# Optimization experiments

Measured on AMD Instinct MI355X. Metric: run time of the kernel, lower is better.

The kernel has to match this reference:

```python
import jax, jax.numpy as jnp
import numpy as np

N_NODES = 50000
N_EDGES = 800000
D_IN = 128
D_OUT = 128
N_MLP = 2


def _lin(x, W, b):
    return x @ W.T + b


def setup_inputs() -> dict:
    key = jax.random.key(0)
    ks = jax.random.split(key, 32)
    d = {}
    d['feat'] = jax.random.normal(ks[0], (N_NODES, D_IN), dtype=jnp.float32)
    d['src'] = jax.random.randint(ks[1], (N_EDGES,), 0, N_NODES, dtype=jnp.int32)
    d['dst'] = jax.random.randint(ks[2], (N_EDGES,), 0, N_NODES, dtype=jnp.int32)
    s_in = 1.0 / np.sqrt(D_IN)
    s_out = 1.0 / np.sqrt(D_OUT)
    i = 3
    def w(shape, s):
        nonlocal i
        out = jax.random.normal(ks[i], shape, dtype=jnp.float32) * s
        i += 1
        return out
    for nm in ['asrc', 'adst', 'asub', 'amul']:
        d['W_' + nm] = w((D_OUT, D_IN), s_in)
        d['b_' + nm] = w((D_OUT,), s_in)
    d['W_aout'] = w((1, D_OUT), s_out)
    d['b_aout'] = w((1,), s_out)
    for nm in ['pool', 'pool2']:
        d['W_' + nm] = w((D_IN, D_IN), s_in)
        d['b_' + nm] = w((D_IN,), s_in)
    for nm in ['self', 'neigh', 'neigh2']:
        d['W_' + nm] = w((D_OUT, D_IN), s_in)
        d['b_' + nm] = w((D_OUT,), s_in)
    d['W_mlp'] = w((N_MLP, D_OUT, D_OUT), s_out)
    d['b_mlp'] = w((N_MLP, D_OUT), s_out)
    return d


def reference(feat, src, dst,
              W_asrc, b_asrc, W_adst, b_adst, W_asub, b_asub, W_amul, b_amul,
              W_aout, b_aout, W_pool, b_pool, W_pool2, b_pool2,
              W_self, b_self, W_neigh, b_neigh, W_neigh2, b_neigh2,
              W_mlp, b_mlp):
    gelu = lambda x: jax.nn.gelu(x, approximate=False)
    fs = feat[src]            # [E, D_IN] gathered source feats
    fd = feat[dst]            # [E, D_IN] gathered dest feats
    # edge attention score
    e = _lin(fs - fd, W_asub, b_asub) + _lin(fs * fd, W_amul, b_amul)
    e = e + _lin(feat, W_asrc, b_asrc)[src] + _lin(feat, W_adst, b_adst)[dst]
    e = gelu(e)
    e = jax.nn.leaky_relu(_lin(e, W_aout, b_aout), 0.2)  # [E, 1]
    deg = jax.ops.segment_sum(jnp.ones((src.shape[0],), jnp.float32), dst,
                              num_segments=N_NODES)      # in-degree
    has_in = (deg > 0)[:, None]
    # max-pool branch
    h = gelu(_lin(feat, W_pool, b_pool))
    m = e * h[src]
    neigh = jax.ops.segment_max(m, dst, num_segments=N_NODES)
    neigh = jnp.where(has_in, neigh, 0.0)
    # mean-pool branch
    h2 = gelu(_lin(feat, W_pool2, b_pool2))
    m2 = e * h2[src]
    neigh2 = jax.ops.segment_sum(m2, dst, num_segments=N_NODES)
    neigh2 = neigh2 / jnp.maximum(deg, 1.0)[:, None]
    rst = _lin(feat, W_self, b_self) + _lin(neigh, W_neigh, b_neigh) \
        + _lin(neigh2, W_neigh2, b_neigh2)
    for li in range(W_mlp.shape[0]):
        rst = rst + _lin(gelu(rst), W_mlp[li], b_mlp[li])
    return rst
```

## Files before the change

### kernel.cpp

```cpp
#include <hip/hip_runtime.h>
#include <cstdint>
#include <cstddef>

#define NN 50000
#define NE 800000
#define DD 128

#define NBK 391
#define BSLOT 4096

static_assert(NN % 16 == 0, "node tiles");
static_assert(NE % 16 == 0, "edge tiles");
static_assert(((NN + 127) >> 7) == NBK, "bucket count");

typedef _Float16 h16_t;
typedef h16_t h16x8 __attribute__((ext_vector_type(8)));
typedef h16_t h16x4 __attribute__((ext_vector_type(4)));
typedef float f32x4 __attribute__((ext_vector_type(4)));
typedef float f32x16 __attribute__((ext_vector_type(16)));

__device__ __forceinline__ float gelu_f(float x) {
    float u = x * x;
    float t = fmaf(u, -0.1029442445f, -2.3021184019f);
    float s = __builtin_amdgcn_exp2f(x * t);
    return x * __builtin_amdgcn_rcpf(1.0f + s);
}

__device__ __forceinline__ int frag_idx(int ch, int k) {
    int t = ch >> 4, n = ch & 15;
    int kb = k >> 5, r = k & 31, q = r >> 3, j = r & 7;
    return ((((t * 4 + kb) * 4 + q) * 16 + n) << 3) + j;
}

__device__ __forceinline__ int frag32_idx(int ch, int k) {
    int t = ch >> 5, m = ch & 31;
    int kc = k >> 4, q = (k >> 3) & 1, j = k & 7;
    return ((((t * 8 + kc) * 2 + q) * 32 + m) << 3) + j;
}

__global__ __launch_bounds__(256) void convert_feat_kernel(
    const float* __restrict__ feat, h16_t* __restrict__ fb)
{
    int i = blockIdx.x * 256 + threadIdx.x;
    f32x4 v = ((const f32x4*)feat)[i];
    h16x4 o;
    o[0] = (h16_t)v[0]; o[1] = (h16_t)v[1]; o[2] = (h16_t)v[2]; o[3] = (h16_t)v[3];
    ((h16x4*)fb)[i] = o;
}

__global__ __launch_bounds__(256) void prep_kernel(
    const float* __restrict__ W_asrc, const float* __restrict__ b_asrc,
    const float* __restrict__ W_adst, const float* __restrict__ b_adst,
    const float* __restrict__ W_asub, const float* __restrict__ b_asub,
    const float* __restrict__ W_amul, const float* __restrict__ b_amul,
    const float* __restrict__ W_pool, const float* __restrict__ W_pool2,
    const float* __restrict__ W_self, const float* __restrict__ b_self,
    const float* __restrict__ W_neigh, const float* __restrict__ b_neigh,
    const float* __restrict__ W_neigh2, const float* __restrict__ b_neigh2,
    const float* __restrict__ W_mlp,
    h16_t* __restrict__ W_Sf, h16_t* __restrict__ W_Df, h16_t* __restrict__ W_amulf,
    h16_t* __restrict__ W_poolf, h16_t* __restrict__ W_pool2f,
    h16_t* __restrict__ W_selff, h16_t* __restrict__ W_neighf, h16_t* __restrict__ W_neigh2f,
    h16_t* __restrict__ W_mlpf,
    float* __restrict__ b_e, float* __restrict__ b_rst)
{
    int gid = blockIdx.x * 256 + threadIdx.x;
    float sub = W_asub[gid];
    int ch = gid >> 7, k = gid & 127;
    int fi = frag_idx(ch, k);
    W_Sf[fi] = (h16_t)(W_asrc[gid] + sub);
    W_Df[fi] = (h16_t)(W_adst[gid] - sub);
    W_amulf[frag32_idx(ch, k)] = (h16_t)W_amul[gid];
    W_poolf[fi]   = (h16_t)W_pool[gid];
    W_pool2f[fi]  = (h16_t)W_pool2[gid];
    W_selff[fi]   = (h16_t)W_self[gid];
    W_neighf[fi]  = (h16_t)W_neigh[gid];
    W_neigh2f[fi] = (h16_t)W_neigh2[gid];
    W_mlpf[fi]            = (h16_t)W_mlp[gid];
    W_mlpf[DD * DD + fi]  = (h16_t)W_mlp[DD * DD + gid];
    if (gid < DD) {
        b_e[gid]   = b_asub[gid] + b_amul[gid] + b_asrc[gid] + b_adst[gid];
        b_rst[gid] = b_self[gid] + b_neigh[gid] + b_neigh2[gid];
    }
}

__global__ __launch_bounds__(256) void scatter_bucket_kernel(
    const int* __restrict__ src, const int* __restrict__ dst,
    int* __restrict__ gcursor, int2* __restrict__ ebuf)
{
    __shared__ int cnt[NBK];
    __shared__ int ofs[NBK];
    int t = threadIdx.x;
    for (int b = t; b < NBK; b += 256) cnt[b] = 0;
    __syncthreads();
    int qbase = blockIdx.x * 1024 + t;
    int4 s4[4], d4[4];
    bool valid[4];
#pragma unroll
    for (int k = 0; k < 4; k++) {
        int q = qbase + k * 256;
        valid[k] = q < NE / 4;
        if (valid[k]) {
            s4[k] = ((const int4*)src)[q];
            d4[k] = ((const int4*)dst)[q];
#pragma unroll
            for (int j = 0; j < 4; j++)
                atomicAdd(&cnt[((&d4[k].x)[j]) >> 7], 1);
        }
    }
    __syncthreads();
    for (int b = t; b < NBK; b += 256) {
        int c = cnt[b];
        ofs[b] = c ? atomicAdd(&gcursor[b], c) : 0;
    }
    __syncthreads();
#pragma unroll
    for (int k = 0; k < 4; k++) {
        if (valid[k]) {
#pragma unroll
            for (int j = 0; j < 4; j++) {
                int d = (&d4[k].x)[j];
                int b = d >> 7;
                int p = atomicAdd(&ofs[b], 1);
                int2 pk;
                pk.x = (&s4[k].x)[j];
                pk.y = d;
                ebuf[(size_t)b * BSLOT + p] = pk;
            }
        }
    }
}

__global__ __launch_bounds__(512) void bucket_scan_kernel(
    const int* __restrict__ gcursor, int* __restrict__ boff)
{
    __shared__ int tmp[512];
    int t = threadIdx.x;
    int v = (t < NBK) ? gcursor[t] : 0;
    tmp[t] = v;
    __syncthreads();
#pragma unroll
    for (int d = 1; d < 512; d <<= 1) {
        int x = (t >= d) ? tmp[t - d] : 0;
        __syncthreads();
        tmp[t] += x;
        __syncthreads();
    }
    if (t < NBK) boff[t] = tmp[t] - v;
}

__global__ __launch_bounds__(256) void finalize_csr_kernel(
    const int2* __restrict__ ebuf, const int* __restrict__ gcursor, const int* __restrict__ boff,
    int2* __restrict__ csr, int* __restrict__ offsets, int* __restrict__ deg)
{
    __shared__ int lcnt[128];
    __shared__ int nbase[128];
    __shared__ int pre[128];
    int B = blockIdx.x, t = threadIdx.x;
    int v0 = B << 7;
    int cnt = gcursor[B];
    int dbase = boff[B];
    const int2* eb = ebuf + (size_t)B * BSLOT;
    if (t < 128) lcnt[t] = 0;
    __syncthreads();
    for (int i = t; i < cnt; i += 256)
        atomicAdd(&lcnt[eb[i].y - v0], 1);
    __syncthreads();
    int c = (t < 128) ? lcnt[t] : 0;
    if (t < 128) pre[t] = c;
    __syncthreads();
#pragma unroll
    for (int d = 1; d < 128; d <<= 1) {
        int x = (t >= d && t < 128) ? pre[t - d] : 0;
        __syncthreads();
        if (t < 128) pre[t] += x;
        __syncthreads();
    }
    if (t < 128) {
        int nb = dbase + pre[t] - c;
        nbase[t] = nb;
        int v = v0 + t;
        if (v < NN) { offsets[v] = nb; deg[v] = c; }
        lcnt[t] = 0;
    }
    __syncthreads();
    for (int i = t; i < cnt; i += 256) {
        int2 pk = eb[i];
        int j = pk.y - v0;
        int pos = nbase[j] + atomicAdd(&lcnt[j], 1);
        csr[pos] = pk;
    }
}

template <bool GELU>
__device__ __forceinline__ void mm16_to_lds(
    const h16x8 a[4], const h16_t* __restrict__ Wf, const float* __restrict__ bias,
    h16_t* __restrict__ L, int n, int q, int lane)
{
#pragma unroll
    for (int t = 0; t < 8; t++) {
        f32x4 acc = {0.f, 0.f, 0.f, 0.f};
#pragma unroll
        for (int kb = 0; kb < 4; kb++) {
            h16x8 b = *(const h16x8*)(Wf + (((t * 4 + kb) * 64 + lane) << 3));
            acc = __builtin_amdgcn_mfma_f32_16x16x32_f16(a[kb], b, acc, 0, 0, 0);
        }
        int ch = t * 16 + n;
        float bv = bias ? bias[ch] : 0.0f;
#pragma unroll
        for (int r = 0; r < 4; r++) {
            float v = acc[r] + bv;
            L[(q * 4 + r) * 136 + ch] = (h16_t)(GELU ? gelu_f(v) : v);
        }
    }
}

__global__ __launch_bounds__(256) void node_linear_kernel(
    const h16_t* __restrict__ fb,
    const h16_t* __restrict__ W_poolf, const float* __restrict__ b_pool,
    const h16_t* __restrict__ W_pool2f, const float* __restrict__ b_pool2,
    const h16_t* __restrict__ W_Sf, const float* __restrict__ b_e,
    const h16_t* __restrict__ W_Df,
    h16_t* __restrict__ hh, h16_t* __restrict__ us, h16_t* __restrict__ ud)
{
    __shared__ __align__(16) h16_t Lh[4][16 * 136];
    __shared__ __align__(16) h16_t Lh2[4][16 * 136];
    int wave = threadIdx.x >> 6;
    int wid = blockIdx.x * 4 + wave;
    if (wid >= NN / 16) return;
    int lane = threadIdx.x & 63, n = lane & 15, q = lane >> 4;
    int nb = wid * 16;
    h16_t* lh = Lh[wave];
    h16_t* lh2 = Lh2[wave];
    h16x8 a[4];
#pragma unroll
    for (int kb = 0; kb < 4; kb++)
        a[kb] = *(const h16x8*)(fb + (size_t)(nb + n) * DD + kb * 32 + q * 8);

    mm16_to_lds<true>(a, W_poolf, b_pool, lh, n, q, lane);
    mm16_to_lds<true>(a, W_pool2f, b_pool2, lh2, n, q, lane);
    __builtin_amdgcn_wave_barrier();
#pragma unroll
    for (int i = 0; i < 8; i++) {
        int r = 2 * i + (lane >> 5);
        int c = lane & 31;
        h16x4 xh = *(const h16x4*)(lh + r * 136 + 4 * c);
        h16x4 x2 = *(const h16x4*)(lh2 + r * 136 + 4 * c);
        h16x8 o;
        o[0] = xh[0]; o[1] = xh[1]; o[2] = x2[0]; o[3] = x2[1];
        o[4] = xh[2]; o[5] = xh[3]; o[6] = x2[2]; o[7] = x2[3];
        *(h16x8*)(hh + (size_t)(nb + r) * 256 + 8 * c) = o;
    }
    __builtin_amdgcn_wave_barrier();
    mm16_to_lds<false>(a, W_Sf, b_e, lh, n, q, lane);
    __builtin_amdgcn_wave_barrier();
#pragma unroll
    for (int i = 0; i < 4; i++) {
        int r = 4 * i + (lane >> 4);
        int c = lane & 15;
        *(h16x8*)(us + (size_t)(nb + r) * 128 + 8 * c) = *(const h16x8*)(lh + r * 136 + 8 * c);
    }
    __builtin_amdgcn_wave_barrier();
    mm16_to_lds<false>(a, W_Df, nullptr, lh, n, q, lane);
    __builtin_amdgcn_wave_barrier();
#pragma unroll
    for (int i = 0; i < 4; i++) {
        int r = 4 * i + (lane >> 4);
        int c = lane & 15;
        *(h16x8*)(ud + (size_t)(nb + r) * 128 + 8 * c) = *(const h16x8*)(lh + r * 136 + 8 * c);
    }
}

#define ES_NBLK 2500
#define ES_ITERS (NE / 32 / ES_NBLK)

__global__ __launch_bounds__(256, 4) void edge_score_kernel(
    const h16_t* __restrict__ fb,
    const h16_t* __restrict__ us, const h16_t* __restrict__ ud,
    const h16_t* __restrict__ W_amulf,
    const float* __restrict__ w_aout, const float* __restrict__ b_aout,
    int2* __restrict__ csr)
{
    __shared__ __align__(16) h16_t sP[32 * 128];
    __shared__ __align__(16) h16_t sU[32 * 128];
    __shared__ float partials[32 * 5];
    __shared__ float sWa[128];
    int tid = threadIdx.x;
    int wave = tid >> 6, lane = tid & 63;
    int n = lane & 31, q = lane >> 5;
    int t = wave;

    if (tid < 128) sWa[tid] = w_aout[tid];

    h16x8 wAm[8];
#pragma unroll
    for (int kc = 0; kc < 8; kc++)
        wAm[kc] = *(const h16x8*)(W_amulf + ((((t * 8 + kc) * 2 + q) * 32 + n) << 3));
    float bout = b_aout[0];

    int sed0 = tid >> 4, sc = tid & 15;

    int e0 = blockIdx.x * 32;
    int2 pk0 = csr[e0 + sed0];
    int2 pk1 = csr[e0 + sed0 + 16];
    h16x8 pfs0 = *(const h16x8*)(fb + (size_t)pk0.x * DD + sc * 8);
    h16x8 pfd0 = *(const h16x8*)(fb + (size_t)pk0.y * DD + sc * 8);
    h16x8 pus0 = *(const h16x8*)(us + (size_t)pk0.x * DD + sc * 8);
    h16x8 pud0 = *(const h16x8*)(ud + (size_t)pk0.y * DD + sc * 8);
    h16x8 pfs1 = *(const h16x8*)(fb + (size_t)pk1.x * DD + sc * 8);
    h16x8 pfd1 = *(const h16x8*)(fb + (size_t)pk1.y * DD + sc * 8);
    h16x8 pus1 = *(const h16x8*)(us + (size_t)pk1.x * DD + sc * 8);
    h16x8 pud1 = *(const h16x8*)(ud + (size_t)pk1.y * DD + sc * 8);

    for (int it = 0; it < ES_ITERS; it++) {
        int eb = (blockIdx.x + it * ES_NBLK) * 32;
        {
            h16x8 pp = pfs0 * pfd0;
            h16x8 uu = pus0 + pud0;
            int ph = (sc ^ (sed0 & 7)) << 3;
            *(h16x8*)(sP + sed0 * 128 + ph) = pp;
            *(h16x8*)(sU + sed0 * 128 + ph) = uu;
        }
        {
            int ed = sed0 + 16;
            h16x8 pp = pfs1 * pfd1;
            h16x8 uu = pus1 + pud1;
            int ph = (sc ^ (ed & 7)) << 3;
            *(h16x8*)(sP + ed * 128 + ph) = pp;
            *(h16x8*)(sU + ed * 128 + ph) = uu;
        }
        __syncthreads();
        if (it + 1 < ES_ITERS) {
            int e1 = (blockIdx.x + (it + 1) * ES_NBLK) * 32;
            pk0 = csr[e1 + sed0];
            pk1 = csr[e1 + sed0 + 16];
            pfs0 = *(const h16x8*)(fb + (size_t)pk0.x * DD + sc * 8);
            pfd0 = *(const h16x8*)(fb + (size_t)pk0.y * DD + sc * 8);
            pus0 = *(const h16x8*)(us + (size_t)pk0.x * DD + sc * 8);
            pud0 = *(const h16x8*)(ud + (size_t)pk0.y * DD + sc * 8);
            pfs1 = *(const h16x8*)(fb + (size_t)pk1.x * DD + sc * 8);
            pfd1 = *(const h16x8*)(fb + (size_t)pk1.y * DD + sc * 8);
            pus1 = *(const h16x8*)(us + (size_t)pk1.x * DD + sc * 8);
            pud1 = *(const h16x8*)(ud + (size_t)pk1.y * DD + sc * 8);
        }
        f32x16 acc = {};
        int swz = n & 7;
#pragma unroll
        for (int kc = 0; kc < 8; kc++) {
            h16x8 bP = *(const h16x8*)(sP + n * 128 + (((kc * 2 + q) ^ swz) << 3));
            acc = __builtin_amdgcn_mfma_f32_32x32x16_f16(wAm[kc], bP, acc, 0, 0, 0);
        }
        float psum = 0.f;
#pragma unroll
        for (int c = 0; c < 4; c++) {
            h16x4 sv = *(const h16x4*)(sU + n * 128 + (((t * 4 + c) ^ swz) << 3) + q * 4);
            f32x4 wv = *(const f32x4*)(sWa + t * 32 + c * 8 + q * 4);
#pragma unroll
            for (int j = 0; j < 4; j++)
                psum = fmaf(gelu_f(acc[c * 4 + j] + (float)sv[j]), wv[j], psum);
        }
        psum += __shfl_xor(psum, 32, 64);
        if (lane < 32) partials[lane * 5 + wave] = psum;
        __syncthreads();
        if (wave == (it & 3) && lane < 32) {
            const float* pr = partials + lane * 5;
            float s = pr[0] + pr[1] + pr[2] + pr[3] + bout;
            s = s > 0.f ? s : 0.2f * s;
            csr[eb + lane].y = __float_as_int(s);
        }
    }
}

__global__ __launch_bounds__(256) void aggregate_kernel(
    const h16_t* __restrict__ hh,
    const int* __restrict__ offsets, const int* __restrict__ deg,
    const int2* __restrict__ csr,
    h16_t* __restrict__ neigh, h16_t* __restrict__ neigh2)
{
    int wave = threadIdx.x >> 6, lane = threadIdx.x & 63;
    int v = blockIdx.x * 4 + wave;
    if (v >= NN) return;
    int off = offsets[v];
    int dg = deg[v];
    int quarter = lane >> 4;
    int cl = lane & 15;
    float mx[8], sm[8];
#pragma unroll
    for (int j = 0; j < 8; j++) { mx[j] = -INFINITY; sm[j] = 0.f; }
    for (int base = 0; base < dg; base += 64) {
        int cnt = dg - base; if (cnt > 64) cnt = 64;
        int s_l = 0; float sc_l = 0.f;
        if (lane < cnt) {
            int2 pk = csr[off + base + lane];
            s_l = pk.x;
            sc_l = __int_as_float(pk.y);
        }
        int nit = (cnt + 3) >> 2;
#pragma unroll 2
        for (int i = 0; i < nit; i++) {
            int idx = 4 * i + quarter;
            int s = __shfl(s_l, idx, 64);
            float sc = __shfl(sc_l, idx, 64);
            if (idx < cnt) {
                const h16_t* row = hh + (size_t)s * 256 + 16 * cl;
                h16x8 h0 = *(const h16x8*)(row);
                h16x8 h1 = *(const h16x8*)(row + 8);
                mx[0] = fmaxf(mx[0], sc * (float)h0[0]);
                mx[1] = fmaxf(mx[1], sc * (float)h0[1]);
                sm[0] = fmaf(sc, (float)h0[2], sm[0]);
                sm[1] = fmaf(sc, (float)h0[3], sm[1]);
                mx[2] = fmaxf(mx[2], sc * (float)h0[4]);
                mx[3] = fmaxf(mx[3], sc * (float)h0[5]);
                sm[2] = fmaf(sc, (float)h0[6], sm[2]);
                sm[3] = fmaf(sc, (float)h0[7], sm[3]);
                mx[4] = fmaxf(mx[4], sc * (float)h1[0]);
                mx[5] = fmaxf(mx[5], sc * (float)h1[1]);
                sm[4] = fmaf(sc, (float)h1[2], sm[4]);
                sm[5] = fmaf(sc, (float)h1[3], sm[5]);
                mx[6] = fmaxf(mx[6], sc * (float)h1[4]);
                mx[7] = fmaxf(mx[7], sc * (float)h1[5]);
                sm[6] = fmaf(sc, (float)h1[6], sm[6]);
                sm[7] = fmaf(sc, (float)h1[7], sm[7]);
            }
        }
    }
#pragma unroll
    for (int j = 0; j < 8; j++) {
        mx[j] = fmaxf(mx[j], __shfl_xor(mx[j], 16, 64));
        mx[j] = fmaxf(mx[j], __shfl_xor(mx[j], 32, 64));
        sm[j] += __shfl_xor(sm[j], 16, 64);
        sm[j] += __shfl_xor(sm[j], 32, 64);
    }
    if (quarter == 0) {
        float inv = 1.0f / (float)(dg > 1 ? dg : 1);
        h16x8 n1, n2;
#pragma unroll
        for (int j = 0; j < 8; j++) {
            n1[j] = (h16_t)(dg > 0 ? mx[j] : 0.0f);
            n2[j] = (h16_t)(sm[j] * inv);
        }
        *(h16x8*)(neigh + (size_t)v * DD + 8 * cl) = n1;
        *(h16x8*)(neigh2 + (size_t)v * DD + 8 * cl) = n2;
    }
}

__global__ __launch_bounds__(256) void final_kernel(
    const h16_t* __restrict__ fb, const h16_t* __restrict__ neigh, const h16_t* __restrict__ neigh2,
    const h16_t* __restrict__ W_selff, const h16_t* __restrict__ W_neighf, const h16_t* __restrict__ W_neigh2f,
    const float* __restrict__ b_rst,
    const h16_t* __restrict__ W_mlpf, const float* __restrict__ b_mlp,
    float* __restrict__ out)
{
    __shared__ __align__(16) float lds[4][16 * 132];
    int wave = threadIdx.x >> 6;
    int wid = blockIdx.x * 4 + wave;
    if (wid >= NN / 16) return;
    int lane = threadIdx.x & 63, n = lane & 15, q = lane >> 4;
    int nb = wid * 16;
    float* L = lds[wave];

    h16x8 af[4], an[4], am[4];
#pragma unroll
    for (int kb = 0; kb < 4; kb++) {
        size_t o = (size_t)(nb + n) * DD + kb * 32 + q * 8;
        af[kb] = *(const h16x8*)(fb + o);
        an[kb] = *(const h16x8*)(neigh + o);
        am[kb] = *(const h16x8*)(neigh2 + o);
    }
    f32x4 rst[8];
#pragma unroll
    for (int t = 0; t < 8; t++) {
        f32x4 acc = {0.f, 0.f, 0.f, 0.f};
#pragma unroll
        for (int kb = 0; kb < 4; kb++) {
            int wo = ((t * 4 + kb) * 64 + lane) << 3;
            acc = __builtin_amdgcn_mfma_f32_16x16x32_f16(af[kb], *(const h16x8*)(W_selff + wo), acc, 0, 0, 0);
            acc = __builtin_amdgcn_mfma_f32_16x16x32_f16(an[kb], *(const h16x8*)(W_neighf + wo), acc, 0, 0, 0);
            acc = __builtin_amdgcn_mfma_f32_16x16x32_f16(am[kb], *(const h16x8*)(W_neigh2f + wo), acc, 0, 0, 0);
        }
        float bv = b_rst[t * 16 + n];
#pragma unroll
        for (int r = 0; r < 4; r++) acc[r] += bv;
        rst[t] = acc;
    }

#pragma unroll
    for (int li = 0; li < 2; li++) {
#pragma unroll
        for (int t = 0; t < 8; t++)
#pragma unroll
            for (int r = 0; r < 4; r++)
                L[(q * 4 + r) * 132 + t * 16 + n] = gelu_f(rst[t][r]);
        __builtin_amdgcn_wave_barrier();
        h16x8 g[4];
#pragma unroll
        for (int kb = 0; kb < 4; kb++) {
            const f32x4* p = (const f32x4*)&L[n * 132 + kb * 32 + q * 8];
            f32x4 x0 = p[0], x1 = p[1];
            h16x8 gg;
            gg[0] = (h16_t)x0[0]; gg[1] = (h16_t)x0[1]; gg[2] = (h16_t)x0[2]; gg[3] = (h16_t)x0[3];
            gg[4] = (h16_t)x1[0]; gg[5] = (h16_t)x1[1]; gg[6] = (h16_t)x1[2]; gg[7] = (h16_t)x1[3];
            g[kb] = gg;
        }
        __builtin_amdgcn_wave_barrier();
        const h16_t* Wl = W_mlpf + li * DD * DD;
#pragma unroll
        for (int t = 0; t < 8; t++) {
            f32x4 acc = {0.f, 0.f, 0.f, 0.f};
#pragma unroll
            for (int kb = 0; kb < 4; kb++) {
                h16x8 b = *(const h16x8*)(Wl + (((t * 4 + kb) * 64 + lane) << 3));
                acc = __builtin_amdgcn_mfma_f32_16x16x32_f16(g[kb], b, acc, 0, 0, 0);
            }
            float bm = b_mlp[li * DD + t * 16 + n];
#pragma unroll
            for (int r = 0; r < 4; r++) rst[t][r] += acc[r] + bm;
        }
    }

#pragma unroll
    for (int t = 0; t < 8; t++)
#pragma unroll
        for (int r = 0; r < 4; r++)
            out[(size_t)(nb + q * 4 + r) * DD + t * 16 + n] = rst[t][r];
}

extern "C" void kernel_launch(void* const* d_in, const int* in_sizes, int n_in,
                              void* d_out, int out_size, void* d_ws, size_t ws_size,
                              hipStream_t stream)
{
    const float* feat    = (const float*)d_in[0];
    const int*   src     = (const int*)d_in[1];
    const int*   dst     = (const int*)d_in[2];
    const float* W_asrc  = (const float*)d_in[3],  *b_asrc  = (const float*)d_in[4];
    const float* W_adst  = (const float*)d_in[5],  *b_adst  = (const float*)d_in[6];
    const float* W_asub  = (const float*)d_in[7],  *b_asub  = (const float*)d_in[8];
    const float* W_amul  = (const float*)d_in[9],  *b_amul  = (const float*)d_in[10];
    const float* W_aout  = (const float*)d_in[11], *b_aout  = (const float*)d_in[12];
    const float* W_pool  = (const float*)d_in[13], *b_pool  = (const float*)d_in[14];
    const float* W_pool2 = (const float*)d_in[15], *b_pool2 = (const float*)d_in[16];
    const float* W_self  = (const float*)d_in[17], *b_self  = (const float*)d_in[18];
    const float* W_neigh = (const float*)d_in[19], *b_neigh = (const float*)d_in[20];
    const float* W_neigh2= (const float*)d_in[21], *b_neigh2= (const float*)d_in[22];
    const float* W_mlp   = (const float*)d_in[23], *b_mlp   = (const float*)d_in[24];
    float* out = (float*)d_out;

    char* w = (char*)d_ws;
    auto take = [&](size_t bytes) -> void* {
        void* p = (void*)w;
        w += (bytes + 255) & ~(size_t)255;
        return p;
    };
    h16_t* fb      = (h16_t*)take((size_t)NN * DD * sizeof(h16_t));
    h16_t* neigh   = (h16_t*)take((size_t)NN * DD * sizeof(h16_t));
    h16_t* neigh2  = (h16_t*)take((size_t)NN * DD * sizeof(h16_t));
    h16_t* hh      = (h16_t*)take((size_t)NN * 256 * sizeof(h16_t));
    h16_t* us      = (h16_t*)take((size_t)NN * DD * sizeof(h16_t));
    h16_t* ud      = (h16_t*)take((size_t)NN * DD * sizeof(h16_t));
    int*    deg     = (int*)take((size_t)NN * sizeof(int));
    int*    offsets = (int*)take((size_t)NN * sizeof(int));
    int2*   csr     = (int2*)take((size_t)NE * sizeof(int2));
    int2*   ebuf    = (int2*)take((size_t)NBK * BSLOT * sizeof(int2));
    int*    gcursor = (int*)take((size_t)NBK * sizeof(int));
    int*    boff    = (int*)take((size_t)NBK * sizeof(int));
    h16_t* W_Sf    = (h16_t*)take((size_t)DD * DD * sizeof(h16_t));
    h16_t* W_Df    = (h16_t*)take((size_t)DD * DD * sizeof(h16_t));
    h16_t* W_amulf = (h16_t*)take((size_t)DD * DD * sizeof(h16_t));
    h16_t* W_poolf = (h16_t*)take((size_t)DD * DD * sizeof(h16_t));
    h16_t* W_pool2f= (h16_t*)take((size_t)DD * DD * sizeof(h16_t));
    h16_t* W_selff = (h16_t*)take((size_t)DD * DD * sizeof(h16_t));
    h16_t* W_neighf= (h16_t*)take((size_t)DD * DD * sizeof(h16_t));
    h16_t* W_neigh2f=(h16_t*)take((size_t)DD * DD * sizeof(h16_t));
    h16_t* W_mlpf  = (h16_t*)take((size_t)2 * DD * DD * sizeof(h16_t));
    float*  b_e     = (float*)take((size_t)DD * sizeof(float));
    float*  b_rst   = (float*)take((size_t)DD * sizeof(float));

    (void)hipMemsetAsync(gcursor, 0, (size_t)NBK * sizeof(int), stream);

    convert_feat_kernel<<<NN * DD / 4 / 256, 256, 0, stream>>>(feat, fb);

    prep_kernel<<<DD * DD / 256, 256, 0, stream>>>(
        W_asrc, b_asrc, W_adst, b_adst, W_asub, b_asub, W_amul, b_amul,
        W_pool, W_pool2, W_self, b_self, W_neigh, b_neigh, W_neigh2, b_neigh2, W_mlp,
        W_Sf, W_Df, W_amulf, W_poolf, W_pool2f, W_selff, W_neighf, W_neigh2f, W_mlpf,
        b_e, b_rst);

    scatter_bucket_kernel<<<(NE / 4 + 1023) / 1024, 256, 0, stream>>>(src, dst, gcursor, ebuf);
    bucket_scan_kernel<<<1, 512, 0, stream>>>(gcursor, boff);
    finalize_csr_kernel<<<NBK, 256, 0, stream>>>(ebuf, gcursor, boff, csr, offsets, deg);

    const int nwaves = NN / 16;
    const int ngrid = (nwaves + 3) / 4;
    node_linear_kernel<<<ngrid, 256, 0, stream>>>(
        fb, W_poolf, b_pool, W_pool2f, b_pool2, W_Sf, b_e, W_Df, hh, us, ud);

    edge_score_kernel<<<ES_NBLK, 256, 0, stream>>>(
        fb, us, ud, W_amulf, W_aout, b_aout, csr);

    aggregate_kernel<<<(NN + 3) / 4, 256, 0, stream>>>(
        hh, offsets, deg, csr, neigh, neigh2);

    final_kernel<<<ngrid, 256, 0, stream>>>(
        fb, neigh, neigh2, W_selff, W_neighf, W_neigh2f, b_rst, W_mlpf, b_mlp, out);
}
```

Measured before the change: 348.7 us.

## Fold bucket scan into CSR finalize and widen edge-score blocks to 64 edges

Removes the separate single-block bucket prefix-scan launch. Each finalize block now computes its own base offset by reducing the counts of all earlier buckets, trading one kernel launch and its serialization for redundant reads in every block. The edge-score kernel moves to 512-thread blocks handling 64 edges per iteration with two wave groups, halving the grid. This amortizes the per-wave weight-register load over more edges and raises work per block, at the cost of larger LDS use and possibly lower occupancy under launch_bounds(512,8).

```diff
diff --git a/kernel.cpp b/kernel.cpp
--- a/kernel.cpp
+++ b/kernel.cpp
@@ -131,35 +131,27 @@
     }
 }
 
-__global__ __launch_bounds__(512) void bucket_scan_kernel(
-    const int* __restrict__ gcursor, int* __restrict__ boff)
-{
-    __shared__ int tmp[512];
-    int t = threadIdx.x;
-    int v = (t < NBK) ? gcursor[t] : 0;
-    tmp[t] = v;
-    __syncthreads();
-#pragma unroll
-    for (int d = 1; d < 512; d <<= 1) {
-        int x = (t >= d) ? tmp[t - d] : 0;
-        __syncthreads();
-        tmp[t] += x;
-        __syncthreads();
-    }
-    if (t < NBK) boff[t] = tmp[t] - v;
-}
-
 __global__ __launch_bounds__(256) void finalize_csr_kernel(
-    const int2* __restrict__ ebuf, const int* __restrict__ gcursor, const int* __restrict__ boff,
+    const int2* __restrict__ ebuf, const int* __restrict__ gcursor,
     int2* __restrict__ csr, int* __restrict__ offsets, int* __restrict__ deg)
 {
     __shared__ int lcnt[128];
     __shared__ int nbase[128];
     __shared__ int pre[128];
+    __shared__ int redbuf[256];
     int B = blockIdx.x, t = threadIdx.x;
     int v0 = B << 7;
     int cnt = gcursor[B];
-    int dbase = boff[B];
+    int partial = 0;
+    for (int i = t; i < B; i += 256) partial += gcursor[i];
+    redbuf[t] = partial;
+    __syncthreads();
+#pragma unroll
+    for (int d = 128; d > 0; d >>= 1) {
+        if (t < d) redbuf[t] += redbuf[t + d];
+        __syncthreads();
+    }
+    int dbase = redbuf[0];
     const int2* eb = ebuf + (size_t)B * BSLOT;
     if (t < 128) lcnt[t] = 0;
     __syncthreads();
@@ -271,24 +263,25 @@
     }
 }
 
-#define ES_NBLK 2500
-#define ES_ITERS (NE / 32 / ES_NBLK)
-
-__global__ __launch_bounds__(256, 4) void edge_score_kernel(
+#define ES_NBLK 1250
+#define ES_ITERS (NE / 64 / ES_NBLK)
+
+__global__ __launch_bounds__(512, 8) void edge_score_kernel(
     const h16_t* __restrict__ fb,
     const h16_t* __restrict__ us, const h16_t* __restrict__ ud,
     const h16_t* __restrict__ W_amulf,
     const float* __restrict__ w_aout, const float* __restrict__ b_aout,
     int2* __restrict__ csr)
 {
-    __shared__ __align__(16) h16_t sP[32 * 128];
-    __shared__ __align__(16) h16_t sU[32 * 128];
-    __shared__ float partials[32 * 5];
+    __shared__ __align__(16) h16_t sP[64 * 128];
+    __shared__ __align__(16) h16_t sU[64 * 128];
+    __shared__ float partials[64 * 5];
     __shared__ float sWa[128];
     int tid = threadIdx.x;
     int wave = tid >> 6, lane = tid & 63;
     int n = lane & 31, q = lane >> 5;
-    int t = wave;
+    int t = wave & 3;
+    int g = wave >> 2;
 
     if (tid < 128) sWa[tid] = w_aout[tid];
 
@@ -298,11 +291,11 @@
         wAm[kc] = *(const h16x8*)(W_amulf + ((((t * 8 + kc) * 2 + q) * 32 + n) << 3));
     float bout = b_aout[0];
 
-    int sed0 = tid >> 4, sc = tid & 15;
-
-    int e0 = blockIdx.x * 32;
-    int2 pk0 = csr[e0 + sed0];
-    int2 pk1 = csr[e0 + sed0 + 16];
+    int sed = tid >> 4, sc = tid & 15;
+
+    int e0 = blockIdx.x * 64;
+    int2 pk0 = csr[e0 + sed];
+    int2 pk1 = csr[e0 + sed + 32];
     h16x8 pfs0 = *(const h16x8*)(fb + (size_t)pk0.x * DD + sc * 8);
     h16x8 pfd0 = *(const h16x8*)(fb + (size_t)pk0.y * DD + sc * 8);
     h16x8 pus0 = *(const h16x8*)(us + (size_t)pk0.x * DD + sc * 8);
@@ -313,16 +306,16 @@
     h16x8 pud1 = *(const h16x8*)(ud + (size_t)pk1.y * DD + sc * 8);
 
     for (int it = 0; it < ES_ITERS; it++) {
-        int eb = (blockIdx.x + it * ES_NBLK) * 32;
+        int eb = (blockIdx.x + it * ES_NBLK) * 64;
         {
             h16x8 pp = pfs0 * pfd0;
             h16x8 uu = pus0 + pud0;
-            int ph = (sc ^ (sed0 & 7)) << 3;
-            *(h16x8*)(sP + sed0 * 128 + ph) = pp;
-            *(h16x8*)(sU + sed0 * 128 + ph) = uu;
+            int ph = (sc ^ (sed & 7)) << 3;
+            *(h16x8*)(sP + sed * 128 + ph) = pp;
+            *(h16x8*)(sU + sed * 128 + ph) = uu;
         }
         {
-            int ed = sed0 + 16;
+            int ed = sed + 32;
             h16x8 pp = pfs1 * pfd1;
             h16x8 uu = pus1 + pud1;
             int ph = (sc ^ (ed & 7)) << 3;
@@ -331,9 +324,9 @@
         }
         __syncthreads();
         if (it + 1 < ES_ITERS) {
-            int e1 = (blockIdx.x + (it + 1) * ES_NBLK) * 32;
-            pk0 = csr[e1 + sed0];
-            pk1 = csr[e1 + sed0 + 16];
+            int e1 = (blockIdx.x + (it + 1) * ES_NBLK) * 64;
+            pk0 = csr[e1 + sed];
+            pk1 = csr[e1 + sed + 32];
             pfs0 = *(const h16x8*)(fb + (size_t)pk0.x * DD + sc * 8);
             pfd0 = *(const h16x8*)(fb + (size_t)pk0.y * DD + sc * 8);
             pus0 = *(const h16x8*)(us + (size_t)pk0.x * DD + sc * 8);
@@ -344,25 +337,26 @@
             pud1 = *(const h16x8*)(ud + (size_t)pk1.y * DD + sc * 8);
         }
         f32x16 acc = {};
+        int row = g * 32 + n;
         int swz = n & 7;
 #pragma unroll
         for (int kc = 0; kc < 8; kc++) {
-            h16x8 bP = *(const h16x8*)(sP + n * 128 + (((kc * 2 + q) ^ swz) << 3));
+            h16x8 bP = *(const h16x8*)(sP + row * 128 + (((kc * 2 + q) ^ swz) << 3));
             acc = __builtin_amdgcn_mfma_f32_32x32x16_f16(wAm[kc], bP, acc, 0, 0, 0);
         }
         float psum = 0.f;
 #pragma unroll
         for (int c = 0; c < 4; c++) {
-            h16x4 sv = *(const h16x4*)(sU + n * 128 + (((t * 4 + c) ^ swz) << 3) + q * 4);
+            h16x4 sv = *(const h16x4*)(sU + row * 128 + (((t * 4 + c) ^ swz) << 3) + q * 4);
             f32x4 wv = *(const f32x4*)(sWa + t * 32 + c * 8 + q * 4);
 #pragma unroll
             for (int j = 0; j < 4; j++)
                 psum = fmaf(gelu_f(acc[c * 4 + j] + (float)sv[j]), wv[j], psum);
         }
         psum += __shfl_xor(psum, 32, 64);
-        if (lane < 32) partials[lane * 5 + wave] = psum;
+        if (lane < 32) partials[(g * 32 + lane) * 5 + t] = psum;
         __syncthreads();
-        if (wave == (it & 3) && lane < 32) {
+        if (wave == (it & 7)) {
             const float* pr = partials + lane * 5;
             float s = pr[0] + pr[1] + pr[2] + pr[3] + bout;
             s = s > 0.f ? s : 0.2f * s;
@@ -562,7 +556,6 @@
     int2*   csr     = (int2*)take((size_t)NE * sizeof(int2));
     int2*   ebuf    = (int2*)take((size_t)NBK * BSLOT * sizeof(int2));
     int*    gcursor = (int*)take((size_t)NBK * sizeof(int));
-    int*    boff    = (int*)take((size_t)NBK * sizeof(int));
     h16_t* W_Sf    = (h16_t*)take((size_t)DD * DD * sizeof(h16_t));
     h16_t* W_Df    = (h16_t*)take((size_t)DD * DD * sizeof(h16_t));
     h16_t* W_amulf = (h16_t*)take((size_t)DD * DD * sizeof(h16_t));
@@ -586,15 +579,14 @@
         b_e, b_rst);
 
     scatter_bucket_kernel<<<(NE / 4 + 1023) / 1024, 256, 0, stream>>>(src, dst, gcursor, ebuf);
-    bucket_scan_kernel<<<1, 512, 0, stream>>>(gcursor, boff);
-    finalize_csr_kernel<<<NBK, 256, 0, stream>>>(ebuf, gcursor, boff, csr, offsets, deg);
+    finalize_csr_kernel<<<NBK, 256, 0, stream>>>(ebuf, gcursor, csr, offsets, deg);
 
     const int nwaves = NN / 16;
     const int ngrid = (nwaves + 3) / 4;
     node_linear_kernel<<<ngrid, 256, 0, stream>>>(
         fb, W_poolf, b_pool, W_pool2f, b_pool2, W_Sf, b_e, W_Df, hh, us, ud);
 
-    edge_score_kernel<<<ES_NBLK, 256, 0, stream>>>(
+    edge_score_kernel<<<ES_NBLK, 512, 0, stream>>>(
         fb, us, ud, W_amulf, W_aout, b_aout, csr);
 
     aggregate_kernel<<<(NN + 3) / 4, 256, 0, stream>>>(
```

Measured after the change: 478.1 us. 37.1% more time.
